# Performance work log

Measured on AMD Instinct MI355X. Metric: run time of the kernel, lower is better.

The kernel has to match this reference:

```python
import jax, jax.numpy as jnp
import numpy as np

DM, DI, DS, DC, DTR, L = 512, 1024, 16, 4, 32, 2
Bb, N = 4, 1024


def layer_norm(x, w, b):
    mu = x.mean(-1, keepdims=True)
    v = ((x - mu) ** 2).mean(-1, keepdims=True)
    return (x - mu) * jax.lax.rsqrt(v + 1e-5) * w + b


def silu(x):
    return x * jax.nn.sigmoid(x)


def selective_ssm(u, p):
    in_w, cw, cb, xpw, dtw, dtb, alog, dd, ow = p
    xz = u @ in_w                        # [B,N,2*DI]
    xh, z = jnp.split(xz, 2, axis=-1)
    # causal depthwise conv over time
    xt = jnp.pad(xh.transpose(0, 2, 1), ((0, 0), (0, 0), (DC - 1, 0)))
    xc = jax.lax.conv_general_dilated(xt, cw[:, None, :], (1,), 'VALID', feature_group_count=DI)
    xh = silu(xc.transpose(0, 2, 1) + cb)
    dbl = xh @ xpw                       # [B,N,DTR+2*DS]
    dt = jax.nn.softplus(dbl[..., :DTR] @ dtw + dtb)   # [B,N,DI]
    Bm = dbl[..., DTR:DTR + DS]
    Cm = dbl[..., DTR + DS:]
    A = -jnp.exp(alog)                   # [DI,DS]

    def step(h, inp):
        dt_t, B_t, C_t, x_t = inp        # [B,DI],[B,DS],[B,DS],[B,DI]
        h = jnp.exp(dt_t[..., None] * A) * h + (dt_t * x_t)[..., None] * B_t[:, None, :]
        return h, jnp.einsum('bds,bs->bd', h, C_t)

    xs = (dt.transpose(1, 0, 2), Bm.transpose(1, 0, 2), Cm.transpose(1, 0, 2), xh.transpose(1, 0, 2))
    h0 = jnp.zeros((u.shape[0], DI, DS), u.dtype)
    _, ys = jax.lax.scan(step, h0, xs)
    y = ys.transpose(1, 0, 2) + dd * xh
    return (y * silu(z)) @ ow


def mamba_layer(h, p):
    n1w, n1b, in_w, cw, cb, xpw, dtw, dtb, alog, dd, ow, n2w, n2b, w1, b1, w2, b2 = p
    h = h + selective_ssm(layer_norm(h, n1w, n1b), (in_w, cw, cb, xpw, dtw, dtb, alog, dd, ow))
    hn = layer_norm(h, n2w, n2b)
    return h + (jax.nn.gelu(hn @ w1 + b1, approximate=False) @ w2 + b2), None


def run_stack(x, stack):
    h, _ = jax.lax.scan(mamba_layer, x, stack)
    return h


def setup_inputs() -> dict:
    key = jax.random.key(0)
    ks = iter(jax.random.split(key, 80))

    def w(shape, s=0.02):
        return jax.random.normal(next(ks), shape, jnp.float32) * s

    d = {"x": jax.random.normal(next(ks), (Bb, N, DM), jnp.float32)}
    for pre in ("f", "b"):
        d[pre + "_n1w"] = jnp.ones((L, DM)); d[pre + "_n1b"] = jnp.zeros((L, DM))
        d[pre + "_inw"] = w((L, DM, 2 * DI)); d[pre + "_cw"] = w((L, DI, DC), 0.1)
        d[pre + "_cb"] = jnp.zeros((L, DI)); d[pre + "_xpw"] = w((L, DI, DTR + 2 * DS))
        d[pre + "_dtw"] = w((L, DTR, DI), 0.1); d[pre + "_dtb"] = w((L, DI), 0.5)
        d[pre + "_alog"] = jnp.tile(jnp.log(jnp.arange(1, DS + 1, dtype=jnp.float32)), (L, DI, 1))
        d[pre + "_dd"] = jnp.ones((L, DI))
        d[pre + "_ow"] = w((L, DI, DM))
        d[pre + "_n2w"] = jnp.ones((L, DM)); d[pre + "_n2b"] = jnp.zeros((L, DM))
        d[pre + "_w1"] = w((L, DM, 4 * DM)); d[pre + "_b1"] = jnp.zeros((L, 4 * DM))
        d[pre + "_w2"] = w((L, 4 * DM, DM)); d[pre + "_b2"] = jnp.zeros((L, DM))
    d["aw1"] = w((DM, DM // 2)); d["ab1"] = jnp.zeros((DM // 2,))
    d["aw2"] = w((DM // 2, 1)); d["ab2"] = jnp.zeros((1,))
    d["nw"] = jnp.ones((2 * DM,)); d["nb"] = jnp.zeros((2 * DM,))
    return d


def reference(x, f_n1w, f_n1b, f_inw, f_cw, f_cb, f_xpw, f_dtw, f_dtb, f_alog, f_dd, f_ow, f_n2w, f_n2b, f_w1, f_b1, f_w2, f_b2, b_n1w, b_n1b, b_inw, b_cw, b_cb, b_xpw, b_dtw, b_dtb, b_alog, b_dd, b_ow, b_n2w, b_n2b, b_w1, b_b1, b_w2, b_b2, aw1, ab1, aw2, ab2, nw, nb):
    fstack = (f_n1w, f_n1b, f_inw, f_cw, f_cb, f_xpw, f_dtw, f_dtb, f_alog, f_dd, f_ow, f_n2w, f_n2b, f_w1, f_b1, f_w2, f_b2)
    bstack = (b_n1w, b_n1b, b_inw, b_cw, b_cb, b_xpw, b_dtw, b_dtb, b_alog, b_dd, b_ow, b_n2w, b_n2b, b_w1, b_b1, b_w2, b_b2)
    hf = run_stack(x, fstack)
    hb = jnp.flip(run_stack(jnp.flip(x, 1), bstack), 1)

    def attn(h):
        return jax.nn.softmax((jnp.tanh(h @ aw1 + ab1) @ aw2 + ab2)[..., 0], axis=-1)

    af = attn(hf)
    abw = attn(hb)
    zf = jnp.einsum('bn,bnd->bd', af, hf)
    zb = jnp.einsum('bn,bnd->bd', abw, hb)
    z = layer_norm(jnp.concatenate([zf, zb], axis=-1), nw, nb)
    return z, (af + abw) * 0.5
```

## Files before the change

### kernel.cpp

```cpp
#include <hip/hip_runtime.h>
#include <math.h>

constexpr int kDM   = 512;
constexpr int kDI   = 1024;
constexpr int kDS   = 16;
constexpr int kDC   = 4;
constexpr int kDTR  = 32;
constexpr int kL    = 2;
constexpr int kB    = 4;
constexpr int kN    = 1024;
constexpr int kB2   = 8;
constexpr int kROWS = kB2 * kN;
constexpr int kMDIR = kB * kN;

enum { EPI_NONE=0, EPI_SOFTPLUS=1, EPI_RESID=2, EPI_GELU=3, EPI_RESID_BIAS=4, EPI_TANH=5 };
enum { MODE_N=0, MODE_OTR=1, MODE_DBL=2, MODE_GATE=3 };

typedef __attribute__((ext_vector_type(8))) short bf16x8;
typedef __attribute__((ext_vector_type(4))) short bf16x4;
typedef __attribute__((ext_vector_type(4))) float f32x4;

__device__ __forceinline__ unsigned short f2bf(float f) {
    unsigned int u = __float_as_uint(f);
    return (unsigned short)((u + 0x7FFFu + ((u >> 16) & 1u)) >> 16);
}
__device__ __forceinline__ float b2f(unsigned short u) {
    return __uint_as_float((unsigned int)u << 16);
}

#define GLD_LDS16(gsrc, ldst) \
    __builtin_amdgcn_global_load_lds((const __attribute__((address_space(1))) void*)(gsrc), \
                                     (__attribute__((address_space(3))) void*)(ldst), 16, 0, 0)

struct WJobs { const float* s[13]; };
constexpr size_t O_INW_F = 0;
constexpr size_t O_INW_B = O_INW_F + 2u*512*2048;
constexpr size_t O_XPW_F = O_INW_B + 2u*512*2048;
constexpr size_t O_XPW_B = O_XPW_F + 2u*1024*64;
constexpr size_t O_DTW_F = O_XPW_B + 2u*1024*64;
constexpr size_t O_DTW_B = O_DTW_F + 2u*32*1024;
constexpr size_t O_OW_F  = O_DTW_B + 2u*32*1024;
constexpr size_t O_OW_B  = O_OW_F  + 2u*1024*512;
constexpr size_t O_W1_F  = O_OW_B  + 2u*1024*512;
constexpr size_t O_W1_B  = O_W1_F  + 2u*512*2048;
constexpr size_t O_W2_F  = O_W1_B  + 2u*512*2048;
constexpr size_t O_W2_B  = O_W2_F  + 2u*2048*512;
constexpr size_t O_AW1   = O_W2_B  + 2u*2048*512;
constexpr size_t O_WTOT  = O_AW1   + 1u*512*256;

__global__ __launch_bounds__(256) void wprep_k(WJobs jobs, unsigned short* __restrict__ dst)
{
    const int wK[13] = {512,512,1024,1024,32,32,1024,1024,512,512,2048,2048,512};
    const int wN[13] = {2048,2048,64,64,1024,1024,512,512,2048,2048,512,512,256};
    const int wL[13] = {2,2,2,2,2,2,2,2,2,2,2,2,1};
    int blk = blockIdx.x;
    int j = 0; int base = 0; size_t doff = 0;
    for (; j < 13; j++) {
        int nb = wL[j] * (wK[j] / 32) * (wN[j] / 32);
        if (blk < base + nb) break;
        base += nb;
        doff += (size_t)wL[j] * wK[j] * wN[j];
    }
    int rel = blk - base;
    int K = wK[j], N = wN[j];
    int tk = K / 32, tn = N / 32;
    int l = rel / (tk * tn); rel -= l * tk * tn;
    int kt = rel / tn, nt = rel - (rel / tn) * tn;
    const float* src = jobs.s[j] + (size_t)l * K * N;
    unsigned short* d = dst + doff + (size_t)l * K * N;
    __shared__ float tl[32][33];
    const int c = threadIdx.x & 31, rg = threadIdx.x >> 5;
#pragma unroll
    for (int rr = 0; rr < 4; rr++)
        tl[rg * 4 + rr][c] = src[(size_t)(kt * 32 + rg * 4 + rr) * N + nt * 32 + c];
    __syncthreads();
#pragma unroll
    for (int rr = 0; rr < 4; rr++)
        d[(size_t)(nt * 32 + rg * 4 + rr) * K + kt * 32 + c] = f2bf(tl[c][rg * 4 + rr]);
}

__global__ __launch_bounds__(256) void init_h_k(const float* __restrict__ x,
                                                float* __restrict__ h)
{
    size_t idx = (size_t)blockIdx.x * 256 + threadIdx.x;
    int d  = idx & (kDM - 1);
    int t  = (idx >> 9) & (kN - 1);
    int bb = (int)(idx >> 19);
    int b = bb & 3, dir = bb >> 2;
    int ts = dir ? (kN - 1 - t) : t;
    h[idx] = x[((size_t)b * kN + ts) * kDM + d];
}

__global__ __launch_bounds__(256) void h2b_k(const float* __restrict__ h,
                                             unsigned short* __restrict__ o)
{
    size_t idx = (size_t)blockIdx.x * 256 + threadIdx.x;
    o[idx] = f2bf(h[idx]);
}

template<int DIM, int OBF>
__global__ __launch_bounds__(256) void ln_k(const float* __restrict__ x,
    const float* __restrict__ wf, const float* __restrict__ wb,
    const float* __restrict__ bf, const float* __restrict__ bbp,
    void* __restrict__ outv)
{
    const int row = blockIdx.x;
    const int tid = threadIdx.x;
    constexpr int PT = DIM / 256;
    const int dir = (row >= kMDIR) ? 1 : 0;
    const float* w = dir ? wb : wf;
    const float* b = dir ? bbp : bf;

    float v[PT];
    float s1 = 0.f, s2 = 0.f;
#pragma unroll
    for (int i = 0; i < PT; i++) {
        float t = x[(size_t)row * DIM + tid + i * 256];
        v[i] = t; s1 += t; s2 += t * t;
    }
    for (int o = 32; o > 0; o >>= 1) { s1 += __shfl_xor(s1, o, 64); s2 += __shfl_xor(s2, o, 64); }
    __shared__ float r1[4], r2[4];
    int wv = tid >> 6;
    if ((tid & 63) == 0) { r1[wv] = s1; r2[wv] = s2; }
    __syncthreads();
    s1 = r1[0] + r1[1] + r1[2] + r1[3];
    s2 = r2[0] + r2[1] + r2[2] + r2[3];
    float mu  = s1 / DIM;
    float var = s2 / DIM - mu * mu;
    float rr  = rsqrtf(var + 1e-5f);
#pragma unroll
    for (int i = 0; i < PT; i++) {
        int c = tid + i * 256;
        float o = (v[i] - mu) * rr * w[c] + b[c];
        if (OBF) ((unsigned short*)outv)[(size_t)row * DIM + c] = f2bf(o);
        else     ((float*)outv)[(size_t)row * DIM + c] = o;
    }
}

template<int BM, int BN, int EPI, int ATR, int MODE, int OBF, int KB>
__global__ __launch_bounds__(256) void gemm_mfma(
    const unsigned short* __restrict__ A, int lda, int K,
    const unsigned short* __restrict__ Btf, const unsigned short* __restrict__ Btb,
    const float* __restrict__ biasf, const float* __restrict__ biasb,
    void* __restrict__ Cv, int ldc, unsigned short* __restrict__ Ct)
{
    constexpr int SK  = 40;
    constexpr int KT  = KB / 32;
    constexpr int CPR = KB / 8;
    constexpr int WM  = BM / 2, WN = BN / 2;
    constexpr int MT  = WM / 16, NT = WN / 16;
    constexpr int ASL = (BM * KB) / (256 * 8);
    constexpr int BSL = (BN * KB) / (256 * 8);
    constexpr int ASZ = (KB == 64) ? BM * 64 : KT * BM * SK;
    constexpr int BSZ = (KB == 64) ? BN * 64 : KT * BN * SK;

    __shared__ __align__(16) unsigned short As[ASZ];
    __shared__ __align__(16) unsigned short Bs[BSZ];

    const int tid  = threadIdx.x;
    const int gx   = gridDim.x;
    const int nwg  = gx * gridDim.y;
    const int lin  = blockIdx.x + blockIdx.y * gx;
    const int swz  = (lin & 7) * (nwg >> 3) + (lin >> 3);
    const int by   = swz / gx;
    const int bx   = swz - by * gx;
    const int n0   = bx * BN;
    const int row0 = by * BM;
    const int dir  = (row0 >= kMDIR) ? 1 : 0;
    const unsigned short* __restrict__ Bt = dir ? Btb : Btf;
    const float* bias = dir ? biasb : biasf;

    const int lane = tid & 63;
    const int wave = tid >> 6;
    const int wr = wave >> 1, wc = wave & 1;
    const int ml = lane & 15, q = lane >> 4;

    f32x4 acc[MT][NT];
#pragma unroll
    for (int i = 0; i < MT; i++)
#pragma unroll
        for (int j = 0; j < NT; j++)
#pragma unroll
            for (int r = 0; r < 4; r++) acc[i][j][r] = 0.f;

    if constexpr (KB == 64) {
        constexpr int ACW = BM / 32;
        constexpr int BCW = BN / 32;
        const int lrow = lane >> 3;
        const int lcol = ((lane & 7) ^ (lrow & 7)) << 4;
        const char* aS[ACW ? ACW : 1];
        const char* bS[BCW ? BCW : 1];
#pragma unroll
        for (int ch = 0; ch < ACW; ch++) {
            const int chunk = wave * ACW + ch;
            aS[ch] = (const char*)A + (size_t)(row0 + chunk * 8 + lrow) * lda * 2 + lcol;
        }
#pragma unroll
        for (int ch = 0; ch < BCW; ch++) {
            const int chunk = wave * BCW + ch;
            bS[ch] = (const char*)Bt + (size_t)(n0 + chunk * 8 + lrow) * K * 2 + lcol;
        }
        const int axor = (ml & 7) << 3;

        for (int kt = 0; kt < K; kt += 64) {
#pragma unroll
            for (int ch = 0; ch < ACW; ch++) {
                GLD_LDS16(aS[ch], &As[(wave * ACW + ch) * 512]);
                aS[ch] += 128;
            }
#pragma unroll
            for (int ch = 0; ch < BCW; ch++) {
                GLD_LDS16(bS[ch], &Bs[(wave * BCW + ch) * 512]);
                bS[ch] += 128;
            }
            __syncthreads();
#pragma unroll
            for (int kk = 0; kk < 2; kk++) {
                bf16x8 af[MT], bfr[NT];
#pragma unroll
                for (int i = 0; i < MT; i++)
                    af[i] = *(bf16x8*)&As[(wr * WM + i * 16 + ml) * 64 + ((kk * 32 + q * 8) ^ axor)];
#pragma unroll
                for (int j = 0; j < NT; j++)
                    bfr[j] = *(bf16x8*)&Bs[(wc * WN + j * 16 + ml) * 64 + ((kk * 32 + q * 8) ^ axor)];
#pragma unroll
                for (int i = 0; i < MT; i++)
#pragma unroll
                    for (int j = 0; j < NT; j++)
                        acc[i][j] = __builtin_amdgcn_mfma_f32_16x16x32_bf16(af[i], bfr[j], acc[i][j], 0, 0, 0);
            }
            __syncthreads();
        }
    } else {
        for (int kt = 0; kt < K; kt += KB) {
            bf16x8 a_ld[ASL ? ASL : 1];
#pragma unroll
            for (int r = 0; r < ASL; r++) {
                int i = tid + r * 256;
                int m = i / CPR, c8 = (i % CPR) * 8;
                a_ld[r] = *(const bf16x8*)(A + (size_t)(row0 + m) * lda + kt + c8);
            }
            bf16x8 b_ld[BSL ? BSL : 1];
#pragma unroll
            for (int r = 0; r < BSL; r++) {
                int i = tid + r * 256;
                int n = i / CPR, c8 = (i % CPR) * 8;
                b_ld[r] = *(const bf16x8*)(Bt + (size_t)(n0 + n) * K + kt + c8);
            }
            __syncthreads();
#pragma unroll
            for (int r = 0; r < ASL; r++) {
                int i = tid + r * 256;
                int m = i / CPR, c8 = (i % CPR) * 8;
                *(bf16x8*)&As[((c8 >> 5) * BM + m) * SK + (c8 & 31)] = a_ld[r];
            }
#pragma unroll
            for (int r = 0; r < BSL; r++) {
                int i = tid + r * 256;
                int n = i / CPR, c8 = (i % CPR) * 8;
                *(bf16x8*)&Bs[((c8 >> 5) * BN + n) * SK + (c8 & 31)] = b_ld[r];
            }
            __syncthreads();
#pragma unroll
            for (int kk = 0; kk < KT; kk++) {
                bf16x8 af[MT], bfr[NT];
#pragma unroll
                for (int i = 0; i < MT; i++)
                    af[i] = *(bf16x8*)&As[(kk * BM + wr * WM + i * 16 + ml) * SK + q * 8];
#pragma unroll
                for (int j = 0; j < NT; j++)
                    bfr[j] = *(bf16x8*)&Bs[(kk * BN + wc * WN + j * 16 + ml) * SK + q * 8];
#pragma unroll
                for (int i = 0; i < MT; i++)
#pragma unroll
                    for (int j = 0; j < NT; j++)
                        acc[i][j] = __builtin_amdgcn_mfma_f32_16x16x32_bf16(af[i], bfr[j], acc[i][j], 0, 0, 0);
            }
            __syncthreads();
        }
    }

    float* Cf = (float*)Cv;
    unsigned short* Cb = (unsigned short*)Cv;
#pragma unroll
    for (int j = 0; j < NT; j++) {
        int col = n0 + wc * WN + j * 16 + ml;
        float bv = 0.f;
        if (EPI == EPI_SOFTPLUS || EPI == EPI_GELU || EPI == EPI_RESID_BIAS || EPI == EPI_TANH)
            bv = bias[col];
#pragma unroll
        for (int i = 0; i < MT; i++) {
            int rw = row0 + wr * WM + i * 16 + q * 4;
            float v4[4];
#pragma unroll
            for (int r = 0; r < 4; r++) {
                float v = acc[i][j][r] + bv;
                if (EPI == EPI_SOFTPLUS) v = (v > 20.f) ? v : __logf(1.f + __expf(v));
                if (EPI == EPI_GELU)     v = 0.5f * v * (1.f + erff(v * 0.70710678118654752f));
                if (EPI == EPI_TANH)     v = tanhf(v);
                v4[r] = v;
            }
            if (MODE == MODE_GATE && n0 >= kDI) {
#pragma unroll
                for (int r = 0; r < 4; r++) {
                    float sv = v4[r] / (1.f + __expf(-v4[r]));
                    Ct[(size_t)(rw + r) * kDI + (col - kDI)] = f2bf(sv);
                }
            } else {
#pragma unroll
                for (int r = 0; r < 4; r++) {
                    size_t o = (size_t)(rw + r) * ldc + col;
                    if (EPI == EPI_RESID || EPI == EPI_RESID_BIAS) Cf[o] += v4[r];
                    else if (OBF) Cb[o] = f2bf(v4[r]);
                    else Cf[o] = v4[r];
                }
                if (MODE == MODE_DBL && col >= 32) {
                    float* F = (float*)Ct;
#pragma unroll
                    for (int r = 0; r < 4; r++)
                        F[(size_t)(rw + r) * 32 + (col - 32)] = v4[r];
                }
            }
        }
    }
}

__global__ __launch_bounds__(256) void conv_k(const unsigned short* __restrict__ xb,
    const float* __restrict__ cwf, const float* __restrict__ cwb,
    const float* __restrict__ cbf, const float* __restrict__ cbb,
    unsigned short* __restrict__ xh)
{
    __shared__ float tl[67][33];
    const int t0 = blockIdx.x * 64, d0 = blockIdx.y * 32, bb = blockIdx.z;
    const int dir = bb >> 2;
    const float* cw = dir ? cwb : cwf;
    const float* cb = dir ? cbb : cbf;
    const int dl = threadIdx.x & 31, rl = threadIdx.x >> 5;
    const size_t base = (size_t)bb * kN * kDI + d0 + dl;
#pragma unroll
    for (int p = 0; p < 9; p++) {
        int r = p * 8 + rl;
        if (r < 67) {
            int ts = t0 + r - 3;
            tl[r][dl] = (ts >= 0) ? b2f(xb[base + (size_t)ts * kDI]) : 0.f;
        }
    }
    __syncthreads();
    const int gd = d0 + dl;
    float c0 = cw[gd*4+0], c1 = cw[gd*4+1], c2 = cw[gd*4+2], c3 = cw[gd*4+3];
    float bv = cb[gd];
#pragma unroll
    for (int jj = 0; jj < 8; jj++) {
        int tt = rl + 8 * jj;
        float acc = bv + c0*tl[tt][dl] + c1*tl[tt+1][dl] + c2*tl[tt+2][dl] + c3*tl[tt+3][dl];
        float o = acc / (1.f + __expf(-acc));
        xh[(size_t)(bb * kN + t0 + tt) * kDI + gd] = f2bf(o);
    }
}

constexpr int kG  = 32;
constexpr int kTg = kN / kG;

template<int PASS>
__global__ __launch_bounds__(256) void bscan_k(
    const unsigned short* __restrict__ dt,
    const unsigned short* __restrict__ xh,
    const unsigned short* __restrict__ gate,
    const float* __restrict__ dblF,
    unsigned short* __restrict__ y,
    float* __restrict__ PL,
    const float* __restrict__ alogf, const float* __restrict__ alogb,
    const float* __restrict__ ddf,   const float* __restrict__ ddb)
{
    const int d  = blockIdx.x * 256 + threadIdx.x;
    const int g  = blockIdx.y;
    const int bb = blockIdx.z;
    const int dir = bb >> 2;
    const float* alog = dir ? alogb : alogf;
    const float* ddp  = dir ? ddb  : ddf;

    float a2[16];
#pragma unroll
    for (int s = 0; s < 16; s += 4) {
        float4 al = *(const float4*)&alog[d * kDS + s];
        a2[s+0] = -__expf(al.x) * 1.44269504f;
        a2[s+1] = -__expf(al.y) * 1.44269504f;
        a2[s+2] = -__expf(al.z) * 1.44269504f;
        a2[s+3] = -__expf(al.w) * 1.44269504f;
    }

    const size_t plb = (size_t)(bb * kG + g) * 32 * kDI + d;
    float h[16];
    if (PASS == 0) {
#pragma unroll
        for (int s = 0; s < 16; s++) h[s] = 0.f;
    } else {
#pragma unroll
        for (int s = 0; s < 16; s++) h[s] = PL[plb + (size_t)(16 + s) * kDI];
    }

    const int row0 = bb * kN + g * kTg;
    const unsigned short* pd = dt   + (size_t)row0 * kDI + d;
    const unsigned short* px = xh   + (size_t)row0 * kDI + d;
    const unsigned short* pg = gate + (size_t)row0 * kDI + d;
    const float* pbc = dblF + (size_t)row0 * 32;
    unsigned short* py = y + (size_t)row0 * kDI + d;
    const float ddv = ddp[d];
    float sdt = 0.f;

#pragma unroll 4
    for (int t = 0; t < kTg; t++) {
        float dtv = b2f(pd[(size_t)t * kDI]);
        float xvv = b2f(px[(size_t)t * kDI]);
        float dtx = dtv * xvv;
        const float* bc = pbc + t * 32;
        if (PASS == 0) {
            sdt += dtv;
#pragma unroll
            for (int s4 = 0; s4 < 4; s4++) {
                float4 Bq = *(const float4*)(bc + s4 * 4);
                h[s4*4+0] = __builtin_amdgcn_exp2f(dtv * a2[s4*4+0]) * h[s4*4+0] + dtx * Bq.x;
                h[s4*4+1] = __builtin_amdgcn_exp2f(dtv * a2[s4*4+1]) * h[s4*4+1] + dtx * Bq.y;
                h[s4*4+2] = __builtin_amdgcn_exp2f(dtv * a2[s4*4+2]) * h[s4*4+2] + dtx * Bq.z;
                h[s4*4+3] = __builtin_amdgcn_exp2f(dtv * a2[s4*4+3]) * h[s4*4+3] + dtx * Bq.w;
            }
        } else {
            float p = 0.f;
#pragma unroll
            for (int s4 = 0; s4 < 4; s4++) {
                float4 Bq = *(const float4*)(bc + s4 * 4);
                float4 Cq = *(const float4*)(bc + 16 + s4 * 4);
                h[s4*4+0] = __builtin_amdgcn_exp2f(dtv * a2[s4*4+0]) * h[s4*4+0] + dtx * Bq.x;
                p += h[s4*4+0] * Cq.x;
                h[s4*4+1] = __builtin_amdgcn_exp2f(dtv * a2[s4*4+1]) * h[s4*4+1] + dtx * Bq.y;
                p += h[s4*4+1] * Cq.y;
                h[s4*4+2] = __builtin_amdgcn_exp2f(dtv * a2[s4*4+2]) * h[s4*4+2] + dtx * Bq.z;
                p += h[s4*4+2] * Cq.z;
                h[s4*4+3] = __builtin_amdgcn_exp2f(dtv * a2[s4*4+3]) * h[s4*4+3] + dtx * Bq.w;
                p += h[s4*4+3] * Cq.w;
            }
            float gvv = b2f(pg[(size_t)t * kDI]);
            py[(size_t)t * kDI] = f2bf((p + ddv * xvv) * gvv);
        }
    }

    if (PASS == 0) {
#pragma unroll
        for (int s = 0; s < 16; s++) {
            PL[plb + (size_t)s * kDI]        = __builtin_amdgcn_exp2f(a2[s] * sdt);
            PL[plb + (size_t)(16 + s) * kDI] = h[s];
        }
    }
}

__global__ __launch_bounds__(256) void bfix_k(float* __restrict__ PL)
{
    const int idx = blockIdx.x * 256 + threadIdx.x;
    const int d  = idx & (kDI - 1);
    const int bb = (idx >> 10) & 7;
    const int s  = idx >> 13;
    float h = 0.f;
    for (int g = 0; g < kG; g++) {
        size_t base = (size_t)(bb * kG + g) * 32 * kDI + d;
        float P = PL[base + (size_t)s * kDI];
        float L = PL[base + (size_t)(16 + s) * kDI];
        PL[base + (size_t)(16 + s) * kDI] = h;
        h = P * h + L;
    }
}

__global__ __launch_bounds__(64) void att_score_k(const unsigned short* __restrict__ tmp,
    const float* __restrict__ aw2, const float* __restrict__ ab2,
    float* __restrict__ score)
{
    int row = blockIdx.x, lane = threadIdx.x;
    float acc = 0.f;
#pragma unroll
    for (int j = 0; j < 4; j++)
        acc += b2f(tmp[(size_t)row * 256 + lane + j * 64]) * aw2[lane + j * 64];
    for (int o = 32; o > 0; o >>= 1) acc += __shfl_xor(acc, o, 64);
    if (lane == 0) score[row] = acc + ab2[0];
}

__global__ __launch_bounds__(256) void softmax_k(const float* __restrict__ score,
                                                 float* __restrict__ w)
{
    int bb = blockIdx.x, tid = threadIdx.x;
    float v[4]; float m = -1e30f;
#pragma unroll
    for (int i = 0; i < 4; i++) { v[i] = score[bb * kN + tid + i * 256]; m = fmaxf(m, v[i]); }
    for (int o = 32; o > 0; o >>= 1) m = fmaxf(m, __shfl_xor(m, o, 64));
    __shared__ float r1[4], r2[4];
    int wv = tid >> 6;
    if ((tid & 63) == 0) r1[wv] = m;
    __syncthreads();
    m = fmaxf(fmaxf(r1[0], r1[1]), fmaxf(r1[2], r1[3]));
    float s = 0.f;
#pragma unroll
    for (int i = 0; i < 4; i++) { v[i] = __expf(v[i] - m); s += v[i]; }
    for (int o = 32; o > 0; o >>= 1) s += __shfl_xor(s, o, 64);
    if ((tid & 63) == 0) r2[wv] = s;
    __syncthreads();
    s = r2[0] + r2[1] + r2[2] + r2[3];
    float inv = 1.f / s;
#pragma unroll
    for (int i = 0; i < 4; i++) w[bb * kN + tid + i * 256] = v[i] * inv;
}

__global__ __launch_bounds__(512) void pool_k(const float* __restrict__ w,
    const float* __restrict__ h, float* zcat)
{
    int bb = blockIdx.x, chunk = blockIdx.y;
    int d = threadIdx.x;
    float acc = 0.f;
    int n0 = chunk * 32;
    for (int n = n0; n < n0 + 32; n++)
        acc += w[bb * kN + n] * h[((size_t)bb * kN + n) * kDM + d];
    int b = bb & 3, dir = bb >> 2;
    atomicAdd(&zcat[b * (2 * kDM) + dir * kDM + d], acc);
}

__global__ __launch_bounds__(256) void att_out_k(const float* __restrict__ w,
                                                 float* __restrict__ out)
{
    int idx = blockIdx.x * 256 + threadIdx.x;
    int b = idx >> 10, n = idx & 1023;
    out[idx] = 0.5f * (w[b * kN + n] + w[(b + 4) * kN + (kN - 1 - n)]);
}

extern "C" void kernel_launch(void* const* d_in, const int* in_sizes, int n_in,
                              void* d_out, int out_size, void* d_ws, size_t ws_size,
                              hipStream_t stream)
{
    const float* x = (const float*)d_in[0];
    const float* fp[17]; const float* bp[17];
    for (int i = 0; i < 17; i++) { fp[i] = (const float*)d_in[1 + i]; bp[i] = (const float*)d_in[18 + i]; }
    const float* aw1 = (const float*)d_in[35];
    const float* ab1 = (const float*)d_in[36];
    const float* aw2 = (const float*)d_in[37];
    const float* ab2 = (const float*)d_in[38];
    const float* nw  = (const float*)d_in[39];
    const float* nb  = (const float*)d_in[40];
    float* out = (float*)d_out;

    float* h = (float*)d_ws;
    unsigned short* ub    = (unsigned short*)(h + (size_t)kROWS * kDM);
    unsigned short* xbuf  = ub    + (size_t)kROWS * kDM;
    unsigned short* tbuf  = xbuf  + (size_t)kROWS * kDI;
    unsigned short* xhb   = tbuf  + (size_t)kROWS * kDI;
    unsigned short* gateb = xhb   + (size_t)kROWS * kDI;
    unsigned short* dbl   = gateb + (size_t)kROWS * kDI;
    float* dblF  = (float*)(dbl + (size_t)kROWS * 64);
    float* score = dblF + (size_t)kROWS * 32;
    float* smw   = score + kROWS;
    float* zcat  = smw   + kROWS;
    unsigned short* wts  = (unsigned short*)(zcat + kB * 2 * kDM);
    float* PL = (float*)(wts + O_WTOT);

    WJobs jobs;
    jobs.s[0] = fp[2];  jobs.s[1] = bp[2];
    jobs.s[2] = fp[5];  jobs.s[3] = bp[5];
    jobs.s[4] = fp[6];  jobs.s[5] = bp[6];
    jobs.s[6] = fp[10]; jobs.s[7] = bp[10];
    jobs.s[8] = fp[13]; jobs.s[9] = bp[13];
    jobs.s[10] = fp[15]; jobs.s[11] = bp[15];
    jobs.s[12] = aw1;
    int wblocks = 0;
    {
        const int wK[13] = {512,512,1024,1024,32,32,1024,1024,512,512,2048,2048,512};
        const int wN[13] = {2048,2048,64,64,1024,1024,512,512,2048,2048,512,512,256};
        const int wL[13] = {2,2,2,2,2,2,2,2,2,2,2,2,1};
        for (int j = 0; j < 13; j++) wblocks += wL[j] * (wK[j]/32) * (wN[j]/32);
    }
    wprep_k<<<wblocks, 256, 0, stream>>>(jobs, wts);

    init_h_k<<<kROWS * kDM / 256, 256, 0, stream>>>(x, h);

    for (int l = 0; l < kL; l++) {
        const float *f_n1w = fp[0]  + l * kDM,            *b_n1w = bp[0]  + l * kDM;
        const float *f_n1b = fp[1]  + l * kDM,            *b_n1b = bp[1]  + l * kDM;
        const float *f_cw  = fp[3]  + l * kDI * kDC,      *b_cw  = bp[3]  + l * kDI * kDC;
        const float *f_cb  = fp[4]  + l * kDI,            *b_cb  = bp[4]  + l * kDI;
        const float *f_dtb = fp[7]  + l * kDI,            *b_dtb = bp[7]  + l * kDI;
        const float *f_alog= fp[8]  + l * kDI * kDS,      *b_alog= bp[8]  + l * kDI * kDS;
        const float *f_dd  = fp[9]  + l * kDI,            *b_dd  = bp[9]  + l * kDI;
        const float *f_n2w = fp[11] + l * kDM,            *b_n2w = bp[11] + l * kDM;
        const float *f_n2b = fp[12] + l * kDM,            *b_n2b = bp[12] + l * kDM;
        const float *f_b1  = fp[14] + l * 4 * kDM,        *b_b1  = bp[14] + l * 4 * kDM;
        const float *f_b2  = fp[16] + l * kDM,            *b_b2  = bp[16] + l * kDM;

        const unsigned short *wInwF = wts + O_INW_F + (size_t)l * 2048 * 512;
        const unsigned short *wInwB = wts + O_INW_B + (size_t)l * 2048 * 512;
        const unsigned short *wXpwF = wts + O_XPW_F + (size_t)l * 64 * 1024;
        const unsigned short *wXpwB = wts + O_XPW_B + (size_t)l * 64 * 1024;
        const unsigned short *wDtwF = wts + O_DTW_F + (size_t)l * 1024 * 32;
        const unsigned short *wDtwB = wts + O_DTW_B + (size_t)l * 1024 * 32;
        const unsigned short *wOwF  = wts + O_OW_F  + (size_t)l * 512 * 1024;
        const unsigned short *wOwB  = wts + O_OW_B  + (size_t)l * 512 * 1024;
        const unsigned short *wW1F  = wts + O_W1_F  + (size_t)l * 2048 * 512;
        const unsigned short *wW1B  = wts + O_W1_B  + (size_t)l * 2048 * 512;
        const unsigned short *wW2F  = wts + O_W2_F  + (size_t)l * 512 * 2048;
        const unsigned short *wW2B  = wts + O_W2_B  + (size_t)l * 512 * 2048;

        ln_k<kDM,1><<<kROWS, 256, 0, stream>>>(h, f_n1w, b_n1w, f_n1b, b_n1b, ub);
        gemm_mfma<128,128,EPI_NONE,0,MODE_GATE,1,64><<<dim3(16, 64), 256, 0, stream>>>(
            ub, kDM, kDM, wInwF, wInwB, nullptr, nullptr, xbuf, kDI, gateb);
        conv_k<<<dim3(kN/64, kDI/32, kB2), 256, 0, stream>>>(
            xbuf, f_cw, b_cw, f_cb, b_cb, xhb);
        gemm_mfma<32,64,EPI_NONE,0,MODE_DBL,1,64><<<dim3(1, 256), 256, 0, stream>>>(
            xhb, kDI, kDI, wXpwF, wXpwB, nullptr, nullptr, dbl, 64, (unsigned short*)dblF);
        gemm_mfma<128,128,EPI_SOFTPLUS,0,MODE_N,1,32><<<dim3(8, 64), 256, 0, stream>>>(
            dbl, 64, kDTR, wDtwF, wDtwB, f_dtb, b_dtb, tbuf, kDI, nullptr);
        bscan_k<0><<<dim3(kDI/256, kG, kB2), 256, 0, stream>>>(
            tbuf, xhb, gateb, dblF, xbuf, PL, f_alog, b_alog, f_dd, b_dd);
        bfix_k<<<kB2 * kDI * kDS / 256, 256, 0, stream>>>(PL);
        bscan_k<1><<<dim3(kDI/256, kG, kB2), 256, 0, stream>>>(
            tbuf, xhb, gateb, dblF, xbuf, PL, f_alog, b_alog, f_dd, b_dd);
        gemm_mfma<128,64,EPI_RESID,0,MODE_N,0,64><<<dim3(8, 64), 256, 0, stream>>>(
            xbuf, kDI, kDI, wOwF, wOwB, nullptr, nullptr, h, kDM, nullptr);
        ln_k<kDM,1><<<kROWS, 256, 0, stream>>>(h, f_n2w, b_n2w, f_n2b, b_n2b, ub);
        gemm_mfma<128,128,EPI_GELU,0,MODE_N,1,64><<<dim3(16, 64), 256, 0, stream>>>(
            ub, kDM, kDM, wW1F, wW1B, f_b1, b_b1, xbuf, 4*kDM, nullptr);
        gemm_mfma<128,64,EPI_RESID_BIAS,0,MODE_N,0,64><<<dim3(8, 64), 256, 0, stream>>>(
            xbuf, 4*kDM, 4*kDM, wW2F, wW2B, f_b2, b_b2, h, kDM, nullptr);
    }

    h2b_k<<<kROWS * kDM / 256, 256, 0, stream>>>(h, tbuf);
    gemm_mfma<64,128,EPI_TANH,0,MODE_N,1,64><<<dim3(2, 128), 256, 0, stream>>>(
        tbuf, kDM, kDM, wts + O_AW1, wts + O_AW1, ab1, ab1, ub, 256, nullptr);
    att_score_k<<<kROWS, 64, 0, stream>>>(ub, aw2, ab2, score);
    softmax_k<<<kB2, 256, 0, stream>>>(score, smw);
    hipMemsetAsync(zcat, 0, kB * 2 * kDM * sizeof(float), stream);
    pool_k<<<dim3(kB2, 32), 512, 0, stream>>>(smw, h, zcat);
    ln_k<2*kDM,0><<<kB, 256, 0, stream>>>(zcat, nw, nw, nb, nb, out);
    att_out_k<<<kB * kN / 256, 256, 0, stream>>>(smw, out + kB * 2 * kDM);
}
```

Before: 711.6 us.

## Double-buffer LDS loads in KB=64 GEMM path and use polynomial erf for GELU

The KB=64 MFMA GEMM path now allocates two LDS buffers and issues the global-to-LDS loads for the next k-tile before computing on the current one. This overlaps memory latency with MFMA work, at the cost of doubling LDS use, which may lower occupancy. Separately, the GELU epilogue swaps erff for an Abramowitz-Stegun polynomial approximation built on hardware rcp and exp2. The polynomial has roughly 1e-7 absolute error, so accuracy changes slightly.

```diff
diff --git a/kernel.cpp b/kernel.cpp
--- a/kernel.cpp
+++ b/kernel.cpp
@@ -26,6 +26,16 @@
 }
 __device__ __forceinline__ float b2f(unsigned short u) {
     return __uint_as_float((unsigned int)u << 16);
+}
+
+__device__ __forceinline__ float erf_as(float x) {
+    float ax = fabsf(x);
+    float t  = __builtin_amdgcn_rcpf(1.f + 0.3275911f * ax);
+    float p  = t * (0.254829592f + t * (-0.284496736f + t * (1.421413741f +
+               t * (-1.453152027f + t * 1.061405429f))));
+    float e  = __builtin_amdgcn_exp2f(ax * ax * -1.44269504f);
+    float r  = 1.f - p * e;
+    return __builtin_copysignf(r, x);
 }
 
 #define GLD_LDS16(gsrc, ldst) \
@@ -151,8 +161,10 @@
     constexpr int MT  = WM / 16, NT = WN / 16;
     constexpr int ASL = (BM * KB) / (256 * 8);
     constexpr int BSL = (BN * KB) / (256 * 8);
-    constexpr int ASZ = (KB == 64) ? BM * 64 : KT * BM * SK;
-    constexpr int BSZ = (KB == 64) ? BN * 64 : KT * BN * SK;
+    constexpr int ABUF = BM * 64;
+    constexpr int BBUF = BN * 64;
+    constexpr int ASZ = (KB == 64) ? 2 * ABUF : KT * BM * SK;
+    constexpr int BSZ = (KB == 64) ? 2 * BBUF : KT * BN * SK;
 
     __shared__ __align__(16) unsigned short As[ASZ];
     __shared__ __align__(16) unsigned short Bs[BSZ];
@@ -202,27 +214,34 @@
         }
         const int axor = (ml & 7) << 3;
 
-        for (int kt = 0; kt < K; kt += 64) {
+        auto stage = [&](int buf) {
 #pragma unroll
             for (int ch = 0; ch < ACW; ch++) {
-                GLD_LDS16(aS[ch], &As[(wave * ACW + ch) * 512]);
+                GLD_LDS16(aS[ch], &As[buf * ABUF + (wave * ACW + ch) * 512]);
                 aS[ch] += 128;
             }
 #pragma unroll
             for (int ch = 0; ch < BCW; ch++) {
-                GLD_LDS16(bS[ch], &Bs[(wave * BCW + ch) * 512]);
+                GLD_LDS16(bS[ch], &Bs[buf * BBUF + (wave * BCW + ch) * 512]);
                 bS[ch] += 128;
             }
-            __syncthreads();
+        };
+
+        stage(0);
+        __syncthreads();
+        const int NKT = K >> 6;
+        int cur = 0;
+        for (int t = 0; t < NKT; t++) {
+            if (t + 1 < NKT) stage(cur ^ 1);
 #pragma unroll
             for (int kk = 0; kk < 2; kk++) {
                 bf16x8 af[MT], bfr[NT];
 #pragma unroll
                 for (int i = 0; i < MT; i++)
-                    af[i] = *(bf16x8*)&As[(wr * WM + i * 16 + ml) * 64 + ((kk * 32 + q * 8) ^ axor)];
+                    af[i] = *(bf16x8*)&As[cur * ABUF + (wr * WM + i * 16 + ml) * 64 + ((kk * 32 + q * 8) ^ axor)];
 #pragma unroll
                 for (int j = 0; j < NT; j++)
-                    bfr[j] = *(bf16x8*)&Bs[(wc * WN + j * 16 + ml) * 64 + ((kk * 32 + q * 8) ^ axor)];
+                    bfr[j] = *(bf16x8*)&Bs[cur * BBUF + (wc * WN + j * 16 + ml) * 64 + ((kk * 32 + q * 8) ^ axor)];
 #pragma unroll
                 for (int i = 0; i < MT; i++)
 #pragma unroll
@@ -230,6 +249,7 @@
                         acc[i][j] = __builtin_amdgcn_mfma_f32_16x16x32_bf16(af[i], bfr[j], acc[i][j], 0, 0, 0);
             }
             __syncthreads();
+            cur ^= 1;
         }
     } else {
         for (int kt = 0; kt < K; kt += KB) {
@@ -296,7 +316,7 @@
             for (int r = 0; r < 4; r++) {
                 float v = acc[i][j][r] + bv;
                 if (EPI == EPI_SOFTPLUS) v = (v > 20.f) ? v : __logf(1.f + __expf(v));
-                if (EPI == EPI_GELU)     v = 0.5f * v * (1.f + erff(v * 0.70710678118654752f));
+                if (EPI == EPI_GELU)     v = 0.5f * v * (1.f + erf_as(v * 0.70710678118654752f));
                 if (EPI == EPI_TANH)     v = tanhf(v);
                 v4[r] = v;
             }
```

New measurement: 685.6 us. -3.6%, faster.
